# Performance work log

Measured on AMD Instinct MI355X. Metric: run time of the kernel, lower is better.

Reference implementation:

```python
import jax, jax.numpy as jnp
import numpy as np

B, H, S, D = 4, 16, 2048, 128

def setup_inputs() -> dict:
    key = jax.random.key(0)
    kq, kk, kv = jax.random.split(key, 3)
    q = jax.random.normal(kq, (B, H, S, D), dtype=jnp.float32)
    k = jax.random.normal(kk, (B, H, S, D), dtype=jnp.float32)
    v = jax.random.normal(kv, (B, H, S, D), dtype=jnp.float32)
    return {"q": q, "k": k, "v": v}

def reference(q, k, v):
    # NOTE: original module applies NO 1/sqrt(d) scale.
    scores = jnp.einsum("bhqd,bhkd->bhqk", q, k)          # [B,H,S,S]
    weights = jax.nn.softmax(scores, axis=-1)
    return jnp.einsum("bhqk,bhkd->bhqd", weights, v)       # [B,H,S,D]
```

## Files before the change

### kernel.cpp

```cpp
#include <hip/hip_runtime.h>
#include <hip/hip_bf16.h>
#include <math.h>
#include <stdint.h>

#define S_LEN 2048
#define D_DIM 128

typedef _Float16 f16x8 __attribute__((ext_vector_type(8)));
typedef __fp16  fp16x2 __attribute__((ext_vector_type(2)));
typedef short bf8_t __attribute__((ext_vector_type(8)));
typedef float f32x4 __attribute__((ext_vector_type(4)));
typedef float f32x16 __attribute__((ext_vector_type(16)));
typedef unsigned int uint32x2 __attribute__((ext_vector_type(2)));
typedef _Float16 f16_t;

__device__ __forceinline__ short f2bf(float f) {
    union { float f; unsigned u; } x; x.f = f;
    unsigned u = x.u;
    u += 0x7FFF + ((u >> 16) & 1);
    return (short)(u >> 16);
}
__device__ __forceinline__ float bf2f(short h) {
    union { unsigned u; float f; } x;
    x.u = ((unsigned)(unsigned short)h) << 16;
    return x.f;
}
__device__ __forceinline__ uint32_t pkf16(float a, float b) {
    union { fp16x2 h; uint32_t u; } x;
    x.h = __builtin_amdgcn_cvt_pkrtz(a, b);
    return x.u;
}
__device__ __forceinline__ uint32x2 plswap(uint32_t a, uint32_t b) {
    return __builtin_amdgcn_permlane32_swap(a, b, false, false);
}
__device__ __forceinline__ float exp2_fast(float x) {
    float r;
    asm("v_exp_f32 %0, %1" : "=v"(r) : "v"(x));
    return r;
}

#define TILE_B 16384
#define WS_VT  33554432u
#define WS_NEED 67108864u

typedef const uint32_t __attribute__((address_space(1))) ga_u32;
typedef uint32_t __attribute__((address_space(3))) la_u32;
__device__ __forceinline__ void gload16(void* l, const void* g) {
    __builtin_amdgcn_global_load_lds((ga_u32*)g, (la_u32*)l, 16, 0, 0);
}

__global__ __launch_bounds__(256, 4)
void conv_kv(const float* __restrict__ K, const float* __restrict__ V,
             char* __restrict__ kf, char* __restrict__ vt)
{
    size_t tile = blockIdx.x;
    const float4* kg = (const float4*)(K + tile * (64 * 128));
    char* kd = kf + tile * TILE_B;
    #pragma unroll
    for (int it = 0; it < 8; ++it) {
        int idx = it * 256 + threadIdx.x;
        int row = idx >> 5;
        int d0  = (idx & 31) * 4;
        float4 kk = kg[idx];
        uint32_t a = pkf16(kk.x, kk.y);
        uint32_t b = pkf16(kk.z, kk.w);
        uint32_t byte = (uint32_t)((row * 256 + d0 * 2) ^ ((row & 7) << 4));
        *(uint32_t*)(kd + byte)     = a;
        *(uint32_t*)(kd + byte + 4) = b;
    }
    const float* vs = V + tile * (64 * 128);
    char* vd = vt + tile * TILE_B;
    #pragma unroll
    for (int it = 0; it < 8; ++it) {
        int idx = it * 256 + threadIdx.x;
        int d  = idx & 127;
        int k0 = (idx >> 7) * 4;
        uint32_t a = pkf16(vs[(k0 + 0) * 128 + d], vs[(k0 + 1) * 128 + d]);
        uint32_t b = pkf16(vs[(k0 + 2) * 128 + d], vs[(k0 + 3) * 128 + d]);
        uint32_t byte = (uint32_t)((d * 128 + k0 * 2) ^ ((d & 7) << 4));
        *(uint32_t*)(vd + byte)     = a;
        *(uint32_t*)(vd + byte + 4) = b;
    }
}

__global__ __launch_bounds__(512, 2)
void attn32(const float* __restrict__ Q, const char* __restrict__ ws,
            float* __restrict__ O)
{
    __shared__ __align__(16) char lds[65536];

    const int tid  = threadIdx.x;
    const int w    = tid >> 6;
    const int lane = tid & 63;
    const int ql   = lane & 31;
    const int h    = lane >> 5;

    const int fid  = blockIdx.x;
    const int nid  = (fid & 7) * 64 + (fid >> 3);
    const int qblk = nid & 7;
    const int bh   = nid >> 3;

    const size_t base = (size_t)bh * S_LEN * D_DIM;
    const int qrow0 = qblk * 256 + w * 32;

    const float L2E = 1.44269504f;
    f16x8 qf[8];
    {
        const float* qp = Q + base + (size_t)(qrow0 + ql) * D_DIM;
        #pragma unroll
        for (int c = 0; c < 8; ++c) {
            const int d0 = c * 16 + h * 8;
            float4 f0 = *(const float4*)(qp + d0);
            float4 f1 = *(const float4*)(qp + d0 + 4);
            qf[c][0] = (f16_t)(f0.x * L2E); qf[c][1] = (f16_t)(f0.y * L2E);
            qf[c][2] = (f16_t)(f0.z * L2E); qf[c][3] = (f16_t)(f0.w * L2E);
            qf[c][4] = (f16_t)(f1.x * L2E); qf[c][5] = (f16_t)(f1.y * L2E);
            qf[c][6] = (f16_t)(f1.z * L2E); qf[c][7] = (f16_t)(f1.w * L2E);
        }
    }

    f32x16 oacc[4];
    #pragma unroll
    for (int nt = 0; nt < 4; ++nt)
        #pragma unroll
        for (int r = 0; r < 16; ++r) oacc[nt][r] = 0.f;
    float m_run = -INFINITY, l_run = 0.f;

    const char* kf_t = ws + (size_t)(bh * 32) * TILE_B;
    const char* vt_t = ws + WS_VT + (size_t)(bh * 32) * TILE_B;
    const int sw = (ql & 7) << 4;

    #pragma unroll
    for (int j = 0; j < 2; ++j) {
        const int off = j * 8192 + w * 1024;
        gload16(lds + off,         kf_t + off + lane * 16);
        gload16(lds + 16384 + off, vt_t + off + lane * 16);
    }
    __syncthreads();

    int bo = 0;
    for (int t6 = 0; t6 < 32; ++t6) {
        if (t6 < 31) {
            const char* kn = kf_t + (size_t)(t6 + 1) * TILE_B;
            const char* vn = vt_t + (size_t)(t6 + 1) * TILE_B;
            const int ob = bo ^ 32768;
            #pragma unroll
            for (int j = 0; j < 2; ++j) {
                const int off = j * 8192 + w * 1024;
                gload16(lds + ob + off,         kn + off + lane * 16);
                gload16(lds + ob + 16384 + off, vn + off + lane * 16);
            }
        }

        f32x16 s0, s1;
        #pragma unroll
        for (int r = 0; r < 16; ++r) { s0[r] = 0.f; s1[r] = 0.f; }
        __builtin_amdgcn_s_setprio(1);
        #pragma unroll
        for (int c = 0; c < 8; ++c) {
            const int b0 = (ql * 256 + c * 32 + h * 16) ^ sw;
            f16x8 a0 = *(const f16x8*)(lds + bo + b0);
            f16x8 a1 = *(const f16x8*)(lds + bo + b0 + 8192);
            s0 = __builtin_amdgcn_mfma_f32_32x32x16_f16(a0, qf[c], s0, 0, 0, 0);
            s1 = __builtin_amdgcn_mfma_f32_32x32x16_f16(a1, qf[c], s1, 0, 0, 0);
        }
        __builtin_amdgcn_s_setprio(0);

        float tm = fmaxf(s0[0], s1[0]);
        #pragma unroll
        for (int r = 1; r < 16; ++r)
            tm = fmaxf(tm, fmaxf(s0[r], s1[r]));
        {
            uint32x2 ts = plswap(__float_as_uint(tm), __float_as_uint(tm));
            tm = fmaxf(__uint_as_float(ts[0]), __uint_as_float(ts[1]));
        }
        if (__any(tm > m_run + 11.f)) {
            const float mn = fmaxf(m_run, tm);
            const float sc = exp2_fast(m_run - mn);
            m_run = mn;
            l_run *= sc;
            #pragma unroll
            for (int r = 0; r < 16; ++r) {
                const float scq = __shfl(sc, (r & 3) + 8 * (r >> 2) + 4 * h);
                oacc[0][r] *= scq; oacc[1][r] *= scq;
                oacc[2][r] *= scq; oacc[3][r] *= scq;
            }
        }
        float ps = 0.f;
        #pragma unroll
        for (int r = 0; r < 16; ++r) {
            float p0 = exp2_fast(s0[r] - m_run); s0[r] = p0; ps += p0;
            float p1 = exp2_fast(s1[r] - m_run); s1[r] = p1; ps += p1;
        }
        {
            uint32x2 pss = plswap(__float_as_uint(ps), __float_as_uint(ps));
            ps = __uint_as_float(pss[0]) + __uint_as_float(pss[1]);
        }
        l_run += ps;

        f16x8 pf[4];
        {
            uint32_t pk[8];
            #pragma unroll
            for (int i = 0; i < 8; ++i) pk[i] = pkf16(s0[2 * i], s0[2 * i + 1]);
            uint32x2 r02 = plswap(pk[0], pk[2]), r13 = plswap(pk[1], pk[3]);
            uint32x2 r46 = plswap(pk[4], pk[6]), r57 = plswap(pk[5], pk[7]);
            union { uint32_t u[4]; f16x8 v; } b0, b1;
            b0.u[0] = r02[0]; b0.u[1] = r13[0]; b0.u[2] = r02[1]; b0.u[3] = r13[1];
            b1.u[0] = r46[0]; b1.u[1] = r57[0]; b1.u[2] = r46[1]; b1.u[3] = r57[1];
            pf[0] = b0.v; pf[1] = b1.v;
        }
        {
            uint32_t pk[8];
            #pragma unroll
            for (int i = 0; i < 8; ++i) pk[i] = pkf16(s1[2 * i], s1[2 * i + 1]);
            uint32x2 r02 = plswap(pk[0], pk[2]), r13 = plswap(pk[1], pk[3]);
            uint32x2 r46 = plswap(pk[4], pk[6]), r57 = plswap(pk[5], pk[7]);
            union { uint32_t u[4]; f16x8 v; } b0, b1;
            b0.u[0] = r02[0]; b0.u[1] = r13[0]; b0.u[2] = r02[1]; b0.u[3] = r13[1];
            b1.u[0] = r46[0]; b1.u[1] = r57[0]; b1.u[2] = r46[1]; b1.u[3] = r57[1];
            pf[2] = b0.v; pf[3] = b1.v;
        }

        __builtin_amdgcn_s_setprio(1);
        #pragma unroll
        for (int nt = 0; nt < 4; ++nt) {
            const int rb = (nt * 32 + ql) * 128;
            #pragma unroll
            for (int kc = 0; kc < 4; ++kc) {
                const int byte = (rb + kc * 32 + h * 16) ^ sw;
                f16x8 vb = *(const f16x8*)(lds + bo + 16384 + byte);
                oacc[nt] = __builtin_amdgcn_mfma_f32_32x32x16_f16(pf[kc], vb, oacc[nt], 0, 0, 0);
            }
        }
        __builtin_amdgcn_s_setprio(0);

        __syncthreads();
        bo ^= 32768;
    }

    const float inv = 1.f / l_run;
    #pragma unroll
    for (int r = 0; r < 16; ++r) {
        const int qr = (r & 3) + 8 * (r >> 2) + 4 * h;
        const float iv = __shfl(inv, qr);
        float* op = O + base + (size_t)(qrow0 + qr) * D_DIM + ql;
        op[0]  = oacc[0][r] * iv;
        op[32] = oacc[1][r] * iv;
        op[64] = oacc[2][r] * iv;
        op[96] = oacc[3][r] * iv;
    }
}

#define PADK 136
#define PADV 72
#define LDS_SHORTS 31232

__global__ __launch_bounds__(256, 2)
void attn_fwd_fb(const float* __restrict__ Q, const float* __restrict__ K,
                 const float* __restrict__ V, float* __restrict__ O)
{
    __shared__ short lds[LDS_SHORTS];
    short* khi = lds;
    short* klo = lds + 8704;
    short* vt  = lds + 17408;
    short* pls = lds + 26624;

    const int tid  = threadIdx.x;
    const int w    = tid >> 6;
    const int lane = tid & 63;
    const int lg   = lane & 15;
    const int gq   = lane >> 4;
    const int qblk = blockIdx.x;
    const int bh   = blockIdx.y;
    const size_t base = (size_t)bh * S_LEN * D_DIM;
    const int qrow0 = qblk * 64 + w * 16;

    bf8_t qhi[4], qlo[4];
    {
        const float* qp = Q + base + (size_t)(qrow0 + lg) * D_DIM;
        #pragma unroll
        for (int c = 0; c < 4; ++c) {
            const int d0 = c * 32 + gq * 8;
            #pragma unroll
            for (int j = 0; j < 8; ++j) {
                float f = qp[d0 + j];
                short hh = f2bf(f);
                qhi[c][j] = hh;
                qlo[c][j] = f2bf(f - bf2f(hh));
            }
        }
    }

    f32x4 oacc[8];
    #pragma unroll
    for (int n = 0; n < 8; ++n) oacc[n] = (f32x4){0.f, 0.f, 0.f, 0.f};
    float mrow[4] = {-INFINITY, -INFINITY, -INFINITY, -INFINITY};
    float lrow[4] = {0.f, 0.f, 0.f, 0.f};

    for (int kv = 0; kv < S_LEN; kv += 64) {
        __syncthreads();
        {
            const float4* kg = (const float4*)(K + base + (size_t)kv * D_DIM);
            const float4* vg = (const float4*)(V + base + (size_t)kv * D_DIM);
            #pragma unroll
            for (int it = 0; it < 8; ++it) {
                const int f4  = it * 256 + tid;
                const int row = f4 >> 5;
                const int d   = (f4 & 31) * 4;
                float4 kk = kg[f4];
                float4 vv = vg[f4];
                short h0 = f2bf(kk.x), h1 = f2bf(kk.y), h2 = f2bf(kk.z), h3 = f2bf(kk.w);
                short4 hw; hw.x = h0; hw.y = h1; hw.z = h2; hw.w = h3;
                *(short4*)(&khi[row * PADK + d]) = hw;
                short4 lw;
                lw.x = f2bf(kk.x - bf2f(h0));
                lw.y = f2bf(kk.y - bf2f(h1));
                lw.z = f2bf(kk.z - bf2f(h2));
                lw.w = f2bf(kk.w - bf2f(h3));
                *(short4*)(&klo[row * PADK + d]) = lw;
                vt[(d + 0) * PADV + row] = f2bf(vv.x);
                vt[(d + 1) * PADV + row] = f2bf(vv.y);
                vt[(d + 2) * PADV + row] = f2bf(vv.z);
                vt[(d + 3) * PADV + row] = f2bf(vv.w);
            }
        }
        __syncthreads();

        f32x4 sacc[4];
        #pragma unroll
        for (int t = 0; t < 4; ++t) sacc[t] = (f32x4){0.f, 0.f, 0.f, 0.f};
        #pragma unroll
        for (int t = 0; t < 4; ++t) {
            const int krow = t * 16 + lg;
            #pragma unroll
            for (int c = 0; c < 4; ++c) {
                bf8_t kh = *(const bf8_t*)(&khi[krow * PADK + c * 32 + gq * 8]);
                bf8_t kl = *(const bf8_t*)(&klo[krow * PADK + c * 32 + gq * 8]);
                sacc[t] = __builtin_amdgcn_mfma_f32_16x16x32_bf16(qhi[c], kh, sacc[t], 0, 0, 0);
                sacc[t] = __builtin_amdgcn_mfma_f32_16x16x32_bf16(qlo[c], kh, sacc[t], 0, 0, 0);
                sacc[t] = __builtin_amdgcn_mfma_f32_16x16x32_bf16(qhi[c], kl, sacc[t], 0, 0, 0);
            }
        }

        float scl[4];
        #pragma unroll
        for (int r = 0; r < 4; ++r) {
            float tm = fmaxf(fmaxf(sacc[0][r], sacc[1][r]),
                             fmaxf(sacc[2][r], sacc[3][r]));
            #pragma unroll
            for (int off = 8; off >= 1; off >>= 1)
                tm = fmaxf(tm, __shfl_xor(tm, off, 64));
            const float mn = fmaxf(mrow[r], tm);
            const float sc = __expf(mrow[r] - mn);
            float ps = 0.f;
            #pragma unroll
            for (int t = 0; t < 4; ++t) {
                float p = __expf(sacc[t][r] - mn);
                sacc[t][r] = p;
                ps += p;
            }
            #pragma unroll
            for (int off = 8; off >= 1; off >>= 1)
                ps += __shfl_xor(ps, off, 64);
            lrow[r] = lrow[r] * sc + ps;
            mrow[r] = mn;
            scl[r] = sc;
        }
        #pragma unroll
        for (int n = 0; n < 8; ++n) {
            oacc[n][0] *= scl[0];
            oacc[n][1] *= scl[1];
            oacc[n][2] *= scl[2];
            oacc[n][3] *= scl[3];
        }

        short* pw = pls + w * (16 * PADV);
        #pragma unroll
        for (int t = 0; t < 4; ++t)
            #pragma unroll
            for (int r = 0; r < 4; ++r)
                pw[(gq * 4 + r) * PADV + t * 16 + lg] = f2bf(sacc[t][r]);
        asm volatile("s_waitcnt lgkmcnt(0)" ::: "memory");

        #pragma unroll
        for (int kt = 0; kt < 2; ++kt) {
            bf8_t pa = *(const bf8_t*)(&pw[lg * PADV + kt * 32 + gq * 8]);
            #pragma unroll
            for (int n = 0; n < 8; ++n) {
                bf8_t vb = *(const bf8_t*)(&vt[(n * 16 + lg) * PADV + kt * 32 + gq * 8]);
                oacc[n] = __builtin_amdgcn_mfma_f32_16x16x32_bf16(pa, vb, oacc[n], 0, 0, 0);
            }
        }
    }

    float inv[4];
    #pragma unroll
    for (int r = 0; r < 4; ++r) inv[r] = 1.f / lrow[r];
    float* op = O + base + (size_t)qrow0 * D_DIM;
    #pragma unroll
    for (int n = 0; n < 8; ++n)
        #pragma unroll
        for (int r = 0; r < 4; ++r)
            op[(size_t)(gq * 4 + r) * D_DIM + n * 16 + lg] = oacc[n][r] * inv[r];
}

extern "C" void kernel_launch(void* const* d_in, const int* in_sizes, int n_in,
                              void* d_out, int out_size, void* d_ws, size_t ws_size,
                              hipStream_t stream) {
    const float* q = (const float*)d_in[0];
    const float* k = (const float*)d_in[1];
    const float* v = (const float*)d_in[2];
    float* o = (float*)d_out;
    if (ws_size >= (size_t)WS_NEED) {
        char* ws = (char*)d_ws;
        conv_kv<<<2048, 256, 0, stream>>>(k, v, ws, ws + WS_VT);
        attn32<<<512, 512, 0, stream>>>(q, ws, o);
    } else {
        attn_fwd_fb<<<dim3(32, 64), 256, 0, stream>>>(q, k, v, o);
    }
}
```

Measured before the change: 220.7 us.

## Triple-buffer K/V tiles in LDS with vmcnt-based waits and one barrier

Switches the K/V staging from double to triple buffering in LDS (96KB). Each iteration now waits only for the oldest tile's loads with a partial vmcnt and one s_barrier, instead of a full __syncthreads after compute. This keeps two tiles in flight to hide global load latency. The cost is more LDS per block, which with launch_bounds(512,2) may limit occupancy to one block per CU, so the occupancy hint could fail.

```diff
diff --git a/kernel.cpp b/kernel.cpp
--- a/kernel.cpp
+++ b/kernel.cpp
@@ -87,7 +87,7 @@
 void attn32(const float* __restrict__ Q, const char* __restrict__ ws,
             float* __restrict__ O)
 {
-    __shared__ __align__(16) char lds[65536];
+    __shared__ __align__(16) char lds[98304];
 
     const int tid  = threadIdx.x;
     const int w    = tid >> 6;
@@ -118,6 +118,7 @@
             qf[c][6] = (f16_t)(f1.z * L2E); qf[c][7] = (f16_t)(f1.w * L2E);
         }
     }
+    asm volatile("s_waitcnt vmcnt(0)" ::: "memory");
 
     f32x16 oacc[4];
     #pragma unroll
@@ -131,25 +132,32 @@
     const int sw = (ql & 7) << 4;
 
     #pragma unroll
-    for (int j = 0; j < 2; ++j) {
-        const int off = j * 8192 + w * 1024;
-        gload16(lds + off,         kf_t + off + lane * 16);
-        gload16(lds + 16384 + off, vt_t + off + lane * 16);
-    }
-    __syncthreads();
-
-    int bo = 0;
+    for (int tt = 0; tt < 2; ++tt) {
+        #pragma unroll
+        for (int j = 0; j < 2; ++j) {
+            const int off = j * 8192 + w * 1024;
+            gload16(lds + tt * 32768 + off,         kf_t + off + lane * 16);
+            gload16(lds + tt * 32768 + 16384 + off, vt_t + off + lane * 16);
+        }
+        kf_t += TILE_B; vt_t += TILE_B;
+    }
+
+    int rdb = 0;
+    int stb = 65536;
     for (int t6 = 0; t6 < 32; ++t6) {
-        if (t6 < 31) {
-            const char* kn = kf_t + (size_t)(t6 + 1) * TILE_B;
-            const char* vn = vt_t + (size_t)(t6 + 1) * TILE_B;
-            const int ob = bo ^ 32768;
+        if (t6 == 31) { asm volatile("s_waitcnt vmcnt(0)" ::: "memory"); }
+        else          { asm volatile("s_waitcnt vmcnt(4)" ::: "memory"); }
+        asm volatile("s_barrier" ::: "memory");
+
+        if (t6 < 30) {
             #pragma unroll
             for (int j = 0; j < 2; ++j) {
                 const int off = j * 8192 + w * 1024;
-                gload16(lds + ob + off,         kn + off + lane * 16);
-                gload16(lds + ob + 16384 + off, vn + off + lane * 16);
-            }
+                gload16(lds + stb + off,         kf_t + off + lane * 16);
+                gload16(lds + stb + 16384 + off, vt_t + off + lane * 16);
+            }
+            kf_t += TILE_B; vt_t += TILE_B;
+            stb = (stb == 65536) ? 0 : stb + 32768;
         }
 
         f32x16 s0, s1;
@@ -159,8 +167,8 @@
         #pragma unroll
         for (int c = 0; c < 8; ++c) {
             const int b0 = (ql * 256 + c * 32 + h * 16) ^ sw;
-            f16x8 a0 = *(const f16x8*)(lds + bo + b0);
-            f16x8 a1 = *(const f16x8*)(lds + bo + b0 + 8192);
+            f16x8 a0 = *(const f16x8*)(lds + rdb + b0);
+            f16x8 a1 = *(const f16x8*)(lds + rdb + b0 + 8192);
             s0 = __builtin_amdgcn_mfma_f32_32x32x16_f16(a0, qf[c], s0, 0, 0, 0);
             s1 = __builtin_amdgcn_mfma_f32_32x32x16_f16(a1, qf[c], s1, 0, 0, 0);
         }
@@ -229,14 +237,13 @@
             #pragma unroll
             for (int kc = 0; kc < 4; ++kc) {
                 const int byte = (rb + kc * 32 + h * 16) ^ sw;
-                f16x8 vb = *(const f16x8*)(lds + bo + 16384 + byte);
+                f16x8 vb = *(const f16x8*)(lds + rdb + 16384 + byte);
                 oacc[nt] = __builtin_amdgcn_mfma_f32_32x32x16_f16(pf[kc], vb, oacc[nt], 0, 0, 0);
             }
         }
         __builtin_amdgcn_s_setprio(0);
 
-        __syncthreads();
-        bo ^= 32768;
+        rdb = (rdb == 65536) ? 0 : rdb + 32768;
     }
 
     const float inv = 1.f / l_run;
```

Result: no change. 221.2 us (+0.3%).
